# Kernel tuning notes

Hardware: AMD Instinct MI355X
Metric: run time of the kernel (lower is better)

## Reference

```python
import jax, jax.numpy as jnp
import numpy as np

B, D, H = 262144, 250, 100  # batch, input_length, hidden_length


def setup_inputs() -> dict:
    key = jax.random.key(0)
    ks = jax.random.split(key, 20)
    s_in = 1.0 / np.sqrt(D)
    s_h = 1.0 / np.sqrt(H)
    inp = {
        "x": jax.random.normal(ks[0], (B, D), jnp.float32),
        "h_prev": jax.random.normal(ks[1], (B, H), jnp.float32),
        "h_shared_prev": jax.random.normal(ks[2], (B, H), jnp.float32),
        # shared nn.GRUCell(D, H) params (torch layout: weight_ih [3H, D], weight_hh [3H, H])
        "Wi": jax.random.uniform(ks[3], (3 * H, D), jnp.float32, -s_in, s_in),
        "Wh": jax.random.uniform(ks[4], (3 * H, H), jnp.float32, -s_h, s_h),
        "bi": jax.random.uniform(ks[5], (3 * H,), jnp.float32, -s_h, s_h),
        "bh": jax.random.uniform(ks[6], (3 * H,), jnp.float32, -s_h, s_h),
        # task-specific bias-free linears, torch nn.Linear layout [out, in]
        "W_z": jax.random.uniform(ks[7], (H, D), jnp.float32, -s_in, s_in),
        "U_z": jax.random.uniform(ks[8], (H, H), jnp.float32, -s_h, s_h),
        "Us_z": jax.random.uniform(ks[9], (H, H), jnp.float32, -s_h, s_h),
        "W_r": jax.random.uniform(ks[10], (H, D), jnp.float32, -s_in, s_in),
        "U_r": jax.random.uniform(ks[11], (H, H), jnp.float32, -s_h, s_h),
        "Us_r": jax.random.uniform(ks[12], (H, H), jnp.float32, -s_h, s_h),
        "W_hn": jax.random.uniform(ks[13], (H, D), jnp.float32, -s_in, s_in),
        "U_hn": jax.random.uniform(ks[14], (H, H), jnp.float32, -s_h, s_h),
        "Us_hn": jax.random.uniform(ks[15], (H, H), jnp.float32, -s_h, s_h),
    }
    return inp


def _shared_gru_cell(x, h, Wi, Wh, bi, bh):
    # standard torch nn.GRUCell math
    gi = x @ Wi.T + bi          # [B, 3H]
    gh = h @ Wh.T + bh          # [B, 3H]
    i_r, i_z, i_n = jnp.split(gi, 3, axis=-1)
    h_r, h_z, h_n = jnp.split(gh, 3, axis=-1)
    r = jax.nn.sigmoid(i_r + h_r)
    z = jax.nn.sigmoid(i_z + h_z)
    n = jnp.tanh(i_n + r * h_n)
    return (1.0 - z) * n + z * h


def reference(x, h_prev, h_shared_prev, Wi, Wh, bi, bh,
              W_z, U_z, Us_z, W_r, U_r, Us_r, W_hn, U_hn, Us_hn):
    h_shared_new = _shared_gru_cell(x, h_shared_prev, Wi, Wh, bi, bh)
    z = jax.nn.sigmoid(x @ W_z.T + h_prev @ U_z.T + h_shared_new @ Us_z.T)
    r = jax.nn.sigmoid(x @ W_r.T + h_prev @ U_r.T + h_shared_new @ Us_r.T)
    nm = jnp.tanh(x @ W_hn.T + r * (h_prev @ U_hn.T) + h_shared_new @ Us_hn.T)
    h_new = (1.0 - z) * nm + z * h_prev
    return h_new
```

## Files before the change

kernel.cpp:

```cpp
#include <hip/hip_runtime.h>
#include <stdint.h>

#define D_IN 250
#define H_DIM 100
#define RPW 32
#define NTHREADS 256
#define BM (4*RPW)

#define P2_FRAG 252
#define TOTAL_E ((252 + 336) * 512)

typedef __bf16 bf16x8 __attribute__((ext_vector_type(8)));
typedef float f32x4 __attribute__((ext_vector_type(4)));

static __device__ __forceinline__ uint16_t f2bf(float f) {
  uint32_t u = __builtin_bit_cast(uint32_t, f);
  u = (u + 0x7FFFu + ((u >> 16) & 1u)) >> 16;
  return (uint16_t)u;
}
static __device__ __forceinline__ float bf2f(uint16_t h) {
  uint32_t u = ((uint32_t)h) << 16;
  return __builtin_bit_cast(float, u);
}
static __device__ __forceinline__ float sigmoidf_(float x) {
  return 1.0f / (1.0f + __expf(-x));
}
static __device__ __forceinline__ float tanhf_(float x) {
  return 2.0f / (1.0f + __expf(-2.0f * x)) - 1.0f;
}

__global__ void prepack_kernel(const float* __restrict__ Wi, const float* __restrict__ Wh,
                               const float* __restrict__ W_z, const float* __restrict__ U_z,
                               const float* __restrict__ Us_z, const float* __restrict__ W_r,
                               const float* __restrict__ U_r, const float* __restrict__ Us_r,
                               const float* __restrict__ W_hn, const float* __restrict__ U_hn,
                               const float* __restrict__ Us_hn, const float* __restrict__ bi,
                               const float* __restrict__ bh, uint16_t* __restrict__ ws) {
  int idx = blockIdx.x * blockDim.x + threadIdx.x;
  if (idx >= TOTAL_E) return;
  int f = idx >> 9;
  int a = idx & 511;
  int lane = a >> 3, j = a & 7;
  int kloc = ((lane >> 4) << 3) + j;
  int cl = lane & 15;
  float val = 0.f;
  if (f < P2_FRAG) {
    int g = f % 3, ks = (f / 3) % 12, t = f / 36;
    int c = t * 16 + cl;
    if (c < H_DIM) {
      if (ks < 8) {
        int k = ks * 32 + kloc;
        if (k < D_IN)       val = Wi[(size_t)(g * H_DIM + c) * D_IN + k];
        else if (k == D_IN) val = bi[g * H_DIM + c];
      } else {
        int k = (ks - 8) * 32 + kloc;
        if (k < H_DIM)       val = Wh[(size_t)(g * H_DIM + c) * H_DIM + k];
        else if (k == H_DIM) val = bh[g * H_DIM + c];
      }
    }
  } else {
    int f2 = f - P2_FRAG;
    int g = f2 % 3, ks = (f2 / 3) % 16, t = f2 / 48;
    int c = t * 16 + cl;
    if (c < H_DIM) {
      if (ks < 8) {
        int k = ks * 32 + kloc;
        const float* W = g == 0 ? W_z : g == 1 ? W_r : W_hn;
        if (k < D_IN) val = W[(size_t)c * D_IN + k];
      } else if (ks < 12) {
        int k = (ks - 8) * 32 + kloc;
        const float* W = g == 0 ? U_z : g == 1 ? U_r : U_hn;
        if (k < H_DIM) val = W[(size_t)c * H_DIM + k];
      } else {
        int k = (ks - 12) * 32 + kloc;
        const float* W = g == 0 ? Us_z : g == 1 ? Us_r : Us_hn;
        if (k < H_DIM) val = W[(size_t)c * H_DIM + k];
      }
    }
  }
  ws[idx] = f2bf(val);
}

static __device__ __forceinline__ bf16x8 xfrag(const float* __restrict__ xr, int ks, int q) {
  int c0 = ks * 32 + q * 8;
  bf16x8 a;
  if (c0 < 248) {
    #pragma unroll
    for (int i = 0; i < 4; ++i) {
      float2 f = *(const float2*)(xr + c0 + 2 * i);
      a[2 * i] = (__bf16)f.x; a[2 * i + 1] = (__bf16)f.y;
    }
  } else {
    float2 f = *(const float2*)(xr + 248);
    a[0] = (__bf16)f.x; a[1] = (__bf16)f.y; a[2] = (__bf16)1.0f;
    a[3] = (__bf16)0.0f; a[4] = (__bf16)0.0f; a[5] = (__bf16)0.0f;
    a[6] = (__bf16)0.0f; a[7] = (__bf16)0.0f;
  }
  return a;
}
static __device__ __forceinline__ bf16x8 hfrag(const float* __restrict__ hr, int ks, int q, float bias) {
  int c0 = ks * 32 + q * 8;
  bf16x8 a;
  #pragma unroll
  for (int i = 0; i < 8; ++i) a[i] = (__bf16)0.0f;
  if (c0 <= 88) {
    #pragma unroll
    for (int i = 0; i < 4; ++i) {
      float2 f = *(const float2*)(hr + c0 + 2 * i);
      a[2 * i] = (__bf16)f.x; a[2 * i + 1] = (__bf16)f.y;
    }
  } else if (c0 == 96) {
    float2 f0 = *(const float2*)(hr + 96);
    float2 f1 = *(const float2*)(hr + 98);
    a[0] = (__bf16)f0.x; a[1] = (__bf16)f0.y; a[2] = (__bf16)f1.x; a[3] = (__bf16)f1.y;
    a[4] = (__bf16)bias;
  }
  return a;
}

#define MFMA(A, B, C) __builtin_amdgcn_mfma_f32_16x16x32_bf16((A), (B), (C), 0, 0, 0)

typedef const __attribute__((address_space(1))) unsigned int* gp1_t;
typedef __attribute__((address_space(3))) unsigned int* lp3_t;

static __device__ __forceinline__ void gload(const uint16_t* gsrc, uint16_t* ldst) {
  __builtin_amdgcn_global_load_lds((gp1_t)gsrc, (lp3_t)ldst, 16, 0, 0);
}
#define WAIT_VM5   asm volatile("s_waitcnt vmcnt(5)" ::: "memory")
#define WAIT_LGKM0 asm volatile("s_waitcnt lgkmcnt(0)" ::: "memory")
#define BAR        do { __builtin_amdgcn_s_barrier(); __builtin_amdgcn_sched_barrier(0); } while (0)

__global__ __launch_bounds__(NTHREADS, 2) void gru_fused(
    const float* __restrict__ x, const float* __restrict__ hp_g,
    const float* __restrict__ hs_g, const uint16_t* __restrict__ ws,
    float* __restrict__ out) {
  __shared__ __align__(16) uint16_t ldsT[4 * RPW * 128];
  __shared__ __align__(16) uint16_t ring[8 * 1536];

  const int tid = threadIdx.x;
  const int lane = tid & 63, wid = tid >> 6;
  const int q = lane >> 4, cl = lane & 15;
  const int rowbase = blockIdx.x * BM + wid * RPW;
  uint16_t* lT = ldsT + wid * (RPW * 128);
  const uint16_t* wsl = ws + lane * 8;

  bf16x8 xa[2][8], ha[2][4], pa[2][4];
  #pragma unroll
  for (int h = 0; h < 2; ++h) {
    const float* xr = x + (size_t)(rowbase + h * 16 + cl) * D_IN;
    #pragma unroll
    for (int ks = 0; ks < 8; ++ks) xa[h][ks] = xfrag(xr, ks, q);
    const float* hr = hs_g + (size_t)(rowbase + h * 16 + cl) * H_DIM;
    #pragma unroll
    for (int ks = 0; ks < 4; ++ks) ha[h][ks] = hfrag(hr, ks, q, 1.0f);
    const float* pr = hp_g + (size_t)(rowbase + h * 16 + cl) * H_DIM;
    #pragma unroll
    for (int ks = 0; ks < 4; ++ks) pa[h][ks] = hfrag(pr, ks, q, 0.0f);
  }

  #pragma unroll
  for (int h = 0; h < 2; ++h) {
    int row = h * 16 + cl;
    #pragma unroll
    for (int ks = 0; ks < 4; ++ks) {
      int bo = row * 256 + (((ks * 64) + q * 16) ^ ((row & 7) << 4));
      *(bf16x8*)((char*)lT + bo) = ha[h][ks];
    }
  }

  if (wid < 3) {
    #pragma unroll
    for (int s = 0; s < 6; ++s)
      gload(wsl + (size_t)(s * 3 + wid) * 512, ring + s * 1536 + wid * 512);
    WAIT_VM5;
  }
  BAR;

  #pragma unroll 1
  for (int t = 0; t < 7; ++t) {
    f32x4 aR[2], aZ[2], aNi[2], aNh[2];
    #pragma unroll
    for (int h = 0; h < 2; ++h) { aR[h] = (f32x4)(0.f); aZ[h] = (f32x4)(0.f); aNi[h] = (f32x4)(0.f); aNh[h] = (f32x4)(0.f); }
    #pragma unroll
    for (int ks = 0; ks < 12; ++ks) {
      const uint16_t* sp = ring + ((t * 12 + ks) & 7) * 1536 + lane * 8;
      bf16x8 b0 = *(const bf16x8*)(sp);
      bf16x8 b1 = *(const bf16x8*)(sp + 512);
      bf16x8 b2 = *(const bf16x8*)(sp + 1024);
      if (wid < 3) {
        int fid = (ks < 6) ? (t * 36 + (ks + 6) * 3)
                : (t < 6 ? ((t + 1) * 36 + (ks - 6) * 3) : (P2_FRAG + (ks - 6) * 3));
        gload(wsl + (size_t)(fid + wid) * 512,
              ring + ((t * 12 + ks + 6) & 7) * 1536 + wid * 512);
      }
      #pragma unroll
      for (int h = 0; h < 2; ++h) {
        bf16x8 av = (ks < 8) ? xa[h][ks] : ha[h][ks - 8];
        aR[h] = MFMA(av, b0, aR[h]);
        aZ[h] = MFMA(av, b1, aZ[h]);
        if (ks < 8) aNi[h] = MFMA(av, b2, aNi[h]);
        else        aNh[h] = MFMA(av, b2, aNh[h]);
      }
      if (wid < 3) WAIT_VM5;
      BAR;
    }
    int c = t * 16 + cl;
    #pragma unroll
    for (int h = 0; h < 2; ++h) {
      #pragma unroll
      for (int r = 0; r < 4; ++r) {
        int row = h * 16 + q * 4 + r;
        int bo = row * 256 + ((c * 2) ^ ((row & 7) << 4));
        float hsp = bf2f(*(const uint16_t*)((const char*)lT + bo));
        float rr = sigmoidf_(aR[h][r]);
        float zz = sigmoidf_(aZ[h][r]);
        float nn = tanhf_(aNi[h][r] + rr * aNh[h][r]);
        float hsn = (1.f - zz) * nn + zz * hsp;
        *(uint16_t*)((char*)lT + bo) = f2bf(hsn);
      }
    }
  }

  bf16x8 na[2][4];
  #pragma unroll
  for (int h = 0; h < 2; ++h) {
    int row = h * 16 + cl;
    #pragma unroll
    for (int ks = 0; ks < 4; ++ks) {
      int bo = row * 256 + (((ks * 64) + q * 16) ^ ((row & 7) << 4));
      na[h][ks] = *(const bf16x8*)((const char*)lT + bo);
    }
  }
  WAIT_LGKM0;
  #pragma unroll
  for (int h = 0; h < 2; ++h) {
    int row = h * 16 + cl;
    #pragma unroll
    for (int ks = 0; ks < 4; ++ks) {
      int bo = row * 256 + (((ks * 64) + q * 16) ^ ((row & 7) << 4));
      *(bf16x8*)((char*)lT + bo) = pa[h][ks];
    }
  }

  #pragma unroll 1
  for (int t = 0; t < 7; ++t) {
    f32x4 aZ[2], aR[2], aNa[2], aNb[2];
    #pragma unroll
    for (int h = 0; h < 2; ++h) { aZ[h] = (f32x4)(0.f); aR[h] = (f32x4)(0.f); aNa[h] = (f32x4)(0.f); aNb[h] = (f32x4)(0.f); }
    #pragma unroll
    for (int ks = 0; ks < 16; ++ks) {
      const uint16_t* sp = ring + ((84 + t * 16 + ks) & 7) * 1536 + lane * 8;
      bf16x8 b0 = *(const bf16x8*)(sp);
      bf16x8 b1 = *(const bf16x8*)(sp + 512);
      bf16x8 b2 = *(const bf16x8*)(sp + 1024);
      if (wid < 3) {
        int fid = (ks < 10) ? (P2_FRAG + t * 48 + (ks + 6) * 3)
                : (t < 6 ? (P2_FRAG + (t + 1) * 48 + (ks - 10) * 3)
                         : (P2_FRAG + 6 * 48 + 15 * 3));
        gload(wsl + (size_t)(fid + wid) * 512,
              ring + ((84 + t * 16 + ks + 6) & 7) * 1536 + wid * 512);
      }
      #pragma unroll
      for (int h = 0; h < 2; ++h) {
        bf16x8 av = (ks < 8) ? xa[h][ks] : (ks < 12) ? pa[h][ks - 8] : na[h][ks - 12];
        aZ[h] = MFMA(av, b0, aZ[h]);
        aR[h] = MFMA(av, b1, aR[h]);
        if (ks < 8)       aNa[h] = MFMA(av, b2, aNa[h]);
        else if (ks < 12) aNb[h] = MFMA(av, b2, aNb[h]);
        else              aNa[h] = MFMA(av, b2, aNa[h]);
      }
      if (wid < 3) WAIT_VM5;
      BAR;
    }
    int c = t * 16 + cl;
    bool valid = c < H_DIM;
    #pragma unroll
    for (int h = 0; h < 2; ++h) {
      #pragma unroll
      for (int r = 0; r < 4; ++r) {
        int row = h * 16 + q * 4 + r;
        int bo = row * 256 + ((c * 2) ^ ((row & 7) << 4));
        float hpv = bf2f(*(const uint16_t*)((const char*)lT + bo));
        float z2 = sigmoidf_(aZ[h][r]);
        float r2 = sigmoidf_(aR[h][r]);
        float nm = tanhf_(aNa[h][r] + r2 * aNb[h][r]);
        float hnew = (1.f - z2) * nm + z2 * hpv;
        if (valid) out[(size_t)(rowbase + row) * H_DIM + c] = hnew;
      }
    }
  }
}

extern "C" void kernel_launch(void* const* d_in, const int* in_sizes, int n_in,
                              void* d_out, int out_size, void* d_ws, size_t ws_size,
                              hipStream_t stream) {
  const float* x    = (const float*)d_in[0];
  const float* h_p  = (const float*)d_in[1];
  const float* h_s  = (const float*)d_in[2];
  const float* Wi   = (const float*)d_in[3];
  const float* Wh   = (const float*)d_in[4];
  const float* bi   = (const float*)d_in[5];
  const float* bh   = (const float*)d_in[6];
  const float* W_z  = (const float*)d_in[7];
  const float* U_z  = (const float*)d_in[8];
  const float* Us_z = (const float*)d_in[9];
  const float* W_r  = (const float*)d_in[10];
  const float* U_r  = (const float*)d_in[11];
  const float* Us_r = (const float*)d_in[12];
  const float* W_hn = (const float*)d_in[13];
  const float* U_hn = (const float*)d_in[14];
  const float* Us_hn= (const float*)d_in[15];
  uint16_t* ws = (uint16_t*)d_ws;
  float* out = (float*)d_out;

  int rows = in_sizes[0] / D_IN;
  prepack_kernel<<<(TOTAL_E + 255) / 256, 256, 0, stream>>>(
      Wi, Wh, W_z, U_z, Us_z, W_r, U_r, Us_r, W_hn, U_hn, Us_hn, bi, bh, ws);
  gru_fused<<<rows / BM, NTHREADS, 0, stream>>>(x, h_p, h_s, ws, out);
}
```

Before: 272.0 us.

## Shrink weight ring to six slots, process two k-steps per barrier, raise MFMA priority

Restructures the LDS weight-streaming pipeline. The ring drops from 8 to 6 slots with prefetch distance 4, and each iteration now handles two k-steps with two global-to-LDS loads, so there are half as many barriers. MFMA sections are wrapped in s_setprio to favour matrix work. This lowers LDS use and cuts sync overhead, at the cost of a shallower prefetch that can expose load latency, plus more complex slot-index arithmetic.

```diff
diff --git a/kernel.cpp b/kernel.cpp
--- a/kernel.cpp
+++ b/kernel.cpp
@@ -9,6 +9,8 @@
 
 #define P2_FRAG 252
 #define TOTAL_E ((252 + 336) * 512)
+
+#define NSLOT 6
 
 typedef __bf16 bf16x8 __attribute__((ext_vector_type(8)));
 typedef float f32x4 __attribute__((ext_vector_type(4)));
@@ -126,7 +128,8 @@
 static __device__ __forceinline__ void gload(const uint16_t* gsrc, uint16_t* ldst) {
   __builtin_amdgcn_global_load_lds((gp1_t)gsrc, (lp3_t)ldst, 16, 0, 0);
 }
-#define WAIT_VM5   asm volatile("s_waitcnt vmcnt(5)" ::: "memory")
+#define WAIT_VM2   asm volatile("s_waitcnt vmcnt(2)" ::: "memory")
+#define WAIT_VM0   asm volatile("s_waitcnt vmcnt(0)" ::: "memory")
 #define WAIT_LGKM0 asm volatile("s_waitcnt lgkmcnt(0)" ::: "memory")
 #define BAR        do { __builtin_amdgcn_s_barrier(); __builtin_amdgcn_sched_barrier(0); } while (0)
 
@@ -135,7 +138,7 @@
     const float* __restrict__ hs_g, const uint16_t* __restrict__ ws,
     float* __restrict__ out) {
   __shared__ __align__(16) uint16_t ldsT[4 * RPW * 128];
-  __shared__ __align__(16) uint16_t ring[8 * 1536];
+  __shared__ __align__(16) uint16_t ring[NSLOT * 1536];
 
   const int tid = threadIdx.x;
   const int lane = tid & 63, wid = tid >> 6;
@@ -170,9 +173,9 @@
 
   if (wid < 3) {
     #pragma unroll
-    for (int s = 0; s < 6; ++s)
+    for (int s = 0; s < 4; ++s)
       gload(wsl + (size_t)(s * 3 + wid) * 512, ring + s * 1536 + wid * 512);
-    WAIT_VM5;
+    WAIT_VM2;
   }
   BAR;
 
@@ -182,26 +185,40 @@
     #pragma unroll
     for (int h = 0; h < 2; ++h) { aR[h] = (f32x4)(0.f); aZ[h] = (f32x4)(0.f); aNi[h] = (f32x4)(0.f); aNh[h] = (f32x4)(0.f); }
     #pragma unroll
-    for (int ks = 0; ks < 12; ++ks) {
-      const uint16_t* sp = ring + ((t * 12 + ks) & 7) * 1536 + lane * 8;
-      bf16x8 b0 = *(const bf16x8*)(sp);
-      bf16x8 b1 = *(const bf16x8*)(sp + 512);
-      bf16x8 b2 = *(const bf16x8*)(sp + 1024);
+    for (int ks = 0; ks < 12; ks += 2) {
+      const uint16_t* sp0 = ring + (ks % NSLOT) * 1536 + lane * 8;
+      const uint16_t* sp1 = ring + ((ks + 1) % NSLOT) * 1536 + lane * 8;
+      bf16x8 a0 = *(const bf16x8*)(sp0);
+      bf16x8 a1 = *(const bf16x8*)(sp0 + 512);
+      bf16x8 a2 = *(const bf16x8*)(sp0 + 1024);
+      bf16x8 b0 = *(const bf16x8*)(sp1);
+      bf16x8 b1 = *(const bf16x8*)(sp1 + 512);
+      bf16x8 b2 = *(const bf16x8*)(sp1 + 1024);
       if (wid < 3) {
-        int fid = (ks < 6) ? (t * 36 + (ks + 6) * 3)
-                : (t < 6 ? ((t + 1) * 36 + (ks - 6) * 3) : (P2_FRAG + (ks - 6) * 3));
-        gload(wsl + (size_t)(fid + wid) * 512,
-              ring + ((t * 12 + ks + 6) & 7) * 1536 + wid * 512);
-      }
+        const int k4 = ks + 4, k5 = ks + 5;
+        int f4 = (k4 < 12) ? (t * 36 + k4 * 3)
+               : (t < 6 ? ((t + 1) * 36 + (k4 - 12) * 3) : (P2_FRAG + (k4 - 12) * 3));
+        int f5 = (k5 < 12) ? (t * 36 + k5 * 3)
+               : (t < 6 ? ((t + 1) * 36 + (k5 - 12) * 3) : (P2_FRAG + (k5 - 12) * 3));
+        gload(wsl + (size_t)(f4 + wid) * 512, ring + (k4 % NSLOT) * 1536 + wid * 512);
+        gload(wsl + (size_t)(f5 + wid) * 512, ring + (k5 % NSLOT) * 1536 + wid * 512);
+      }
+      __builtin_amdgcn_s_setprio(1);
       #pragma unroll
       for (int h = 0; h < 2; ++h) {
-        bf16x8 av = (ks < 8) ? xa[h][ks] : ha[h][ks - 8];
-        aR[h] = MFMA(av, b0, aR[h]);
-        aZ[h] = MFMA(av, b1, aZ[h]);
-        if (ks < 8) aNi[h] = MFMA(av, b2, aNi[h]);
-        else        aNh[h] = MFMA(av, b2, aNh[h]);
-      }
-      if (wid < 3) WAIT_VM5;
+        bf16x8 av0 = (ks < 8) ? xa[h][ks] : ha[h][ks - 8];
+        aR[h] = MFMA(av0, a0, aR[h]);
+        aZ[h] = MFMA(av0, a1, aZ[h]);
+        if (ks < 8) aNi[h] = MFMA(av0, a2, aNi[h]);
+        else        aNh[h] = MFMA(av0, a2, aNh[h]);
+        bf16x8 av1 = (ks + 1 < 8) ? xa[h][ks + 1] : ha[h][ks + 1 - 8];
+        aR[h] = MFMA(av1, b0, aR[h]);
+        aZ[h] = MFMA(av1, b1, aZ[h]);
+        if (ks + 1 < 8) aNi[h] = MFMA(av1, b2, aNi[h]);
+        else            aNh[h] = MFMA(av1, b2, aNh[h]);
+      }
+      __builtin_amdgcn_s_setprio(0);
+      if (wid < 3) WAIT_VM2;
       BAR;
     }
     int c = t * 16 + cl;
@@ -242,34 +259,53 @@
     }
   }
 
+  int sb = 0;
   #pragma unroll 1
   for (int t = 0; t < 7; ++t) {
     f32x4 aZ[2], aR[2], aNa[2], aNb[2];
     #pragma unroll
     for (int h = 0; h < 2; ++h) { aZ[h] = (f32x4)(0.f); aR[h] = (f32x4)(0.f); aNa[h] = (f32x4)(0.f); aNb[h] = (f32x4)(0.f); }
     #pragma unroll
-    for (int ks = 0; ks < 16; ++ks) {
-      const uint16_t* sp = ring + ((84 + t * 16 + ks) & 7) * 1536 + lane * 8;
-      bf16x8 b0 = *(const bf16x8*)(sp);
-      bf16x8 b1 = *(const bf16x8*)(sp + 512);
-      bf16x8 b2 = *(const bf16x8*)(sp + 1024);
+    for (int ks = 0; ks < 16; ks += 2) {
+      int s0 = sb + (ks % NSLOT);          if (s0 >= NSLOT) s0 -= NSLOT;
+      int s1 = sb + ((ks + 1) % NSLOT);    if (s1 >= NSLOT) s1 -= NSLOT;
+      const uint16_t* sp0 = ring + s0 * 1536 + lane * 8;
+      const uint16_t* sp1 = ring + s1 * 1536 + lane * 8;
+      bf16x8 a0 = *(const bf16x8*)(sp0);
+      bf16x8 a1 = *(const bf16x8*)(sp0 + 512);
+      bf16x8 a2 = *(const bf16x8*)(sp0 + 1024);
+      bf16x8 b0 = *(const bf16x8*)(sp1);
+      bf16x8 b1 = *(const bf16x8*)(sp1 + 512);
+      bf16x8 b2 = *(const bf16x8*)(sp1 + 1024);
       if (wid < 3) {
-        int fid = (ks < 10) ? (P2_FRAG + t * 48 + (ks + 6) * 3)
-                : (t < 6 ? (P2_FRAG + (t + 1) * 48 + (ks - 10) * 3)
-                         : (P2_FRAG + 6 * 48 + 15 * 3));
-        gload(wsl + (size_t)(fid + wid) * 512,
-              ring + ((84 + t * 16 + ks + 6) & 7) * 1536 + wid * 512);
-      }
+        const int k4 = ks + 4, k5 = ks + 5;
+        int f4 = (k4 < 16) ? (P2_FRAG + t * 48 + k4 * 3)
+               : (t < 6 ? (P2_FRAG + (t + 1) * 48 + (k4 - 16) * 3) : P2_FRAG);
+        int f5 = (k5 < 16) ? (P2_FRAG + t * 48 + k5 * 3)
+               : (t < 6 ? (P2_FRAG + (t + 1) * 48 + (k5 - 16) * 3) : P2_FRAG);
+        int s4 = sb + (k4 % NSLOT);        if (s4 >= NSLOT) s4 -= NSLOT;
+        int s5 = sb + (k5 % NSLOT);        if (s5 >= NSLOT) s5 -= NSLOT;
+        gload(wsl + (size_t)(f4 + wid) * 512, ring + s4 * 1536 + wid * 512);
+        gload(wsl + (size_t)(f5 + wid) * 512, ring + s5 * 1536 + wid * 512);
+      }
+      __builtin_amdgcn_s_setprio(1);
       #pragma unroll
       for (int h = 0; h < 2; ++h) {
-        bf16x8 av = (ks < 8) ? xa[h][ks] : (ks < 12) ? pa[h][ks - 8] : na[h][ks - 12];
-        aZ[h] = MFMA(av, b0, aZ[h]);
-        aR[h] = MFMA(av, b1, aR[h]);
-        if (ks < 8)       aNa[h] = MFMA(av, b2, aNa[h]);
-        else if (ks < 12) aNb[h] = MFMA(av, b2, aNb[h]);
-        else              aNa[h] = MFMA(av, b2, aNa[h]);
-      }
-      if (wid < 3) WAIT_VM5;
+        bf16x8 av0 = (ks < 8) ? xa[h][ks] : (ks < 12) ? pa[h][ks - 8] : na[h][ks - 12];
+        aZ[h] = MFMA(av0, a0, aZ[h]);
+        aR[h] = MFMA(av0, a1, aR[h]);
+        if (ks < 8)       aNa[h] = MFMA(av0, a2, aNa[h]);
+        else if (ks < 12) aNb[h] = MFMA(av0, a2, aNb[h]);
+        else              aNa[h] = MFMA(av0, a2, aNa[h]);
+        bf16x8 av1 = (ks + 1 < 8) ? xa[h][ks + 1] : (ks + 1 < 12) ? pa[h][ks + 1 - 8] : na[h][ks + 1 - 12];
+        aZ[h] = MFMA(av1, b0, aZ[h]);
+        aR[h] = MFMA(av1, b1, aR[h]);
+        if (ks + 1 < 8)       aNa[h] = MFMA(av1, b2, aNa[h]);
+        else if (ks + 1 < 12) aNb[h] = MFMA(av1, b2, aNb[h]);
+        else                  aNa[h] = MFMA(av1, b2, aNa[h]);
+      }
+      __builtin_amdgcn_s_setprio(0);
+      if (wid < 3) WAIT_VM2;
       BAR;
     }
     int c = t * 16 + cl;
@@ -288,7 +324,11 @@
         if (valid) out[(size_t)(rowbase + row) * H_DIM + c] = hnew;
       }
     }
-  }
+    sb += 4;
+    if (sb >= NSLOT) sb -= NSLOT;
+  }
+
+  WAIT_VM0;
 }
 
 extern "C" void kernel_launch(void* const* d_in, const int* in_sizes, int n_in,
```

Measured after the change: 270.4 us. About the same (-0.6%).
